# Performance work log

Measured on AMD Instinct MI355X. Metric: run time of the kernel, lower is better.

Reference implementation:

```python
import jax, jax.numpy as jnp
import numpy as np

B, C, H, W = 32, 320, 64, 64
CTX_DIM, CTX_HW = 1024, 16


def _conv3x3(x, w, b):
    # x: [b, cin, h, w], w: [cout, cin, 3, 3] (OIHW), stride 1, SAME padding
    y = jax.lax.conv_general_dilated(x, w, window_strides=(1, 1), padding='SAME',
                                     dimension_numbers=('NCHW', 'OIHW', 'NCHW'))
    return y + b[None, :, None, None]


def setup_inputs() -> dict:
    key = jax.random.key(0)
    ks = jax.random.split(key, 8)
    global_x = jax.random.normal(ks[0], (B, C, H, W), jnp.float32)
    context = jax.random.normal(ks[1], (B, CTX_HW * CTX_HW, CTX_DIM), jnp.float32)
    indicator = jax.random.randint(ks[2], (B, 2), 0, 2).astype(jnp.float32)
    # bbox = (x1, y1, x2, y2) normalized; keep boxes inside [0,1) so no sample
    # hits the torch try/except skip path, but sizes vary per sample.
    lo = jax.random.uniform(ks[3], (B, 2), minval=0.0, maxval=0.4)
    ext = jax.random.uniform(ks[4], (B, 2), minval=0.1, maxval=0.55)
    bbox = jnp.concatenate([lo, lo + ext], axis=1)
    # params (local_proj_out is zero-init in the source; we use small random
    # weights so the baseline is non-degenerate)
    w_in = jax.random.normal(ks[5], (C, CTX_DIM + 2, 3, 3), jnp.float32) * 0.02
    b_in = jnp.zeros((C,), jnp.float32)
    w_out = jax.random.normal(ks[6], (C, C, 3, 3), jnp.float32) * 0.02
    b_out = jnp.zeros((C,), jnp.float32)
    return {'global_x': global_x, 'context': context, 'indicator': indicator,
            'bbox': bbox, 'w_in': w_in, 'b_in': b_in, 'w_out': w_out, 'b_out': b_out}


def reference(global_x, context, indicator, bbox, w_in, b_in, w_out, b_out):
    b, c, h, w = global_x.shape
    # 'b (h w) c -> b c h w' with h=16
    ctx = context.reshape(b, CTX_HW, CTX_HW, -1).transpose(0, 3, 1, 2)
    ind_map = jnp.broadcast_to(indicator[:, :, None, None], (b, 2, CTX_HW, CTX_HW))
    ctx = jnp.concatenate([ctx, ind_map], axis=1)  # [b, ctx_dim+2, 16, 16]
    cx = _conv3x3(ctx, w_in, b_in)
    cx = cx * jax.nn.sigmoid(cx)                    # silu
    cx = _conv3x3(cx, w_out, b_out)                 # [b, c, 16, 16]
    # per-sample ROI nearest-resize + add, fully vectorized (torch loop body)
    bb = (bbox * h).astype(jnp.int32)               # truncation like .int()
    x1, y1 = bb[:, 0], bb[:, 1]
    x2 = jnp.maximum(bb[:, 2], x1 + 1)
    y2 = jnp.maximum(bb[:, 3], y1 + 1)
    # torch try/except skips samples where slice shapes mismatch (box off-grid)
    ok = (y2 <= h) & (x2 <= w) & (y1 >= 0) & (x1 >= 0)
    ys = jnp.arange(h)[None, :]
    xs = jnp.arange(w)[None, :]
    # nearest interpolation: src = floor(dst * in_size / out_size)
    src_y = jnp.clip(((ys - y1[:, None]) * CTX_HW) // (y2 - y1)[:, None], 0, CTX_HW - 1)
    src_x = jnp.clip(((xs - x1[:, None]) * CTX_HW) // (x2 - x1)[:, None], 0, CTX_HW - 1)
    vy = (ys >= y1[:, None]) & (ys < y2[:, None])   # [b, h]
    vx = (xs >= x1[:, None]) & (xs < x2[:, None])   # [b, w]
    bi = jnp.arange(b)[:, None, None]
    # gather per output pixel -> [b, h, w, c] -> [b, c, h, w]
    local = cx[bi, :, src_y[:, :, None], src_x[:, None, :]].transpose(0, 3, 1, 2)
    mask = (ok[:, None, None] & vy[:, :, None] & vx[:, None, :])[:, None]  # [b,1,h,w]
    return global_x + jnp.where(mask, local, jnp.zeros((), global_x.dtype))
```

## Files before the change

kernel.cpp:

```cpp
#include <hip/hip_runtime.h>
#include <cstddef>

#define BB 32
#define CC 320
#define HH 64
#define WW 64
#define CTX_HW 16
#define NPIX 256

typedef __attribute__((ext_vector_type(8))) short bf16x8;
typedef __attribute__((ext_vector_type(4))) float f32x4;

__device__ inline ushort f2bf(float x) {
  union { float f; unsigned u; } v; v.f = x;
  unsigned r = v.u + 0x7fff + ((v.u >> 16) & 1);
  return (ushort)(r >> 16);
}

__global__ __launch_bounds__(256) void cast_ctx(
    const float* __restrict__ ctx, const float* __restrict__ ind,
    ushort* __restrict__ ctxP, ushort* __restrict__ cx1P) {
  int b = blockIdx.x, p = blockIdx.y, t = threadIdx.x;
  ushort* orow = ctxP + ((size_t)b * 257 + p) * 1056;
  if (p < 256) {
    const float* irow = ctx + ((size_t)b * 256 + p) * 1024;
    float4 v = ((const float4*)irow)[t];
    ushort4 o;
    o.x = f2bf(v.x); o.y = f2bf(v.y); o.z = f2bf(v.z); o.w = f2bf(v.w);
    ((ushort4*)orow)[t] = o;
    if (t < 32) {
      float val = (t == 0) ? ind[b * 2] : (t == 1) ? ind[b * 2 + 1] : 0.0f;
      orow[1024 + t] = f2bf(val);
    }
  } else {
    ushort4 z = make_ushort4(0, 0, 0, 0);
    for (int i = t; i < 264; i += 256) ((ushort4*)orow)[i] = z;
    if (t < 80) ((ushort4*)(cx1P + ((size_t)b * 257 + 256) * 320))[t] = z;
  }
}

template <int KIN, int KP>
__global__ __launch_bounds__(256) void wt_tr(
    const float* __restrict__ w, ushort* __restrict__ wT) {
  __shared__ float wl[KIN * 9];
  int co = blockIdx.x, t = threadIdx.x;
  const float* wsrc = w + (size_t)co * KIN * 9;
  for (int i = t; i < KIN * 9; i += 256) wl[i] = wsrc[i];
  __syncthreads();
#pragma unroll
  for (int tap = 0; tap < 9; ++tap) {
    ushort* dst = wT + ((size_t)tap * 320 + co) * KP;
    for (int ci = t; ci < KP; ci += 256)
      dst[ci] = f2bf(ci < KIN ? wl[ci * 9 + tap] : 0.0f);
  }
}

__global__ __launch_bounds__(64) void prep_maps(
    const float* __restrict__ bbox, int* __restrict__ sy, int* __restrict__ sx) {
  int b = blockIdx.x;
  int t = threadIdx.x;
  int x1 = (int)(bbox[b * 4 + 0] * (float)HH);
  int y1 = (int)(bbox[b * 4 + 1] * (float)HH);
  int x2 = max((int)(bbox[b * 4 + 2] * (float)HH), x1 + 1);
  int y2 = max((int)(bbox[b * 4 + 3] * (float)HH), y1 + 1);
  bool ok = (y2 <= HH) && (x2 <= WW) && (y1 >= 0) && (x1 >= 0);
  int vy = -1, vx = -1;
  if (ok && t >= y1 && t < y2) vy = min(15, max(0, ((t - y1) * CTX_HW) / (y2 - y1)));
  if (ok && t >= x1 && t < x2) vx = min(15, max(0, ((t - x1) * CTX_HW) / (x2 - x1)));
  sy[b * 64 + t] = vy;
  sx[b * 64 + t] = vx;
}

template <int KP, int NCH, int KS>
__global__ __launch_bounds__(512, 4) void conv_part(
    const ushort* __restrict__ src, const ushort* __restrict__ wT,
    float* __restrict__ part) {
  constexpr int PL = 40;
  __shared__ ushort plane[257 * PL];

  int b = blockIdx.x;
  int co0 = blockIdx.y * 64;
  int z = blockIdx.z;
  int c0 = z * NCH / KS, c1 = (z + 1) * NCH / KS;
  int tid = threadIdx.x;
  int wid = tid >> 6, lane = tid & 63;
  int m = lane & 15, quad = lane >> 4;
  int mg = wid >> 1, ng = wid & 1;
  int y0 = mg * 4;
  int coA = co0 + ng * 32 + m;

  if (tid < PL) plane[256 * PL + tid] = 0;

  f32x4 acc[4][2];
#pragma unroll
  for (int i = 0; i < 4; ++i) {
    acc[i][0] = (f32x4)(0.0f);
    acc[i][1] = (f32x4)(0.0f);
  }

  const ushort* srcb = src + (size_t)b * 257 * KP;
  int row = tid >> 1, half = tid & 1;
  const ushort* gsrc = srcb + (size_t)row * KP + half * 16;
  ushort* lds_dst = plane + row * PL + half * 16;

  for (int cic = c0; cic < c1; ++cic) {
    __syncthreads();
    {
      const float4* g = (const float4*)(gsrc + cic * 32);
      float4 v0 = g[0];
      float4 v1 = g[1];
      ((float4*)lds_dst)[0] = v0;
      ((float4*)lds_dst)[1] = v1;
    }
    __syncthreads();
    const ushort* wb0 = wT + (size_t)coA * KP + cic * 32 + quad * 8;
    const ushort* wb1 = wb0 + (size_t)16 * KP;
#pragma unroll
    for (int dx = 0; dx < 3; ++dx) {
      int sxp = m + dx - 1;
      bool vx = (unsigned)sxp < 16u;
      bf16x8 af[6];
#pragma unroll
      for (int j = 0; j < 6; ++j) {
        int syr = y0 - 1 + j;
        bool v = vx && ((unsigned)syr < 16u);
        int ldsrow = v ? (syr * 16 + sxp) : 256;
        af[j] = *(const bf16x8*)(plane + ldsrow * PL + quad * 8);
      }
#pragma unroll
      for (int dy = 0; dy < 3; ++dy) {
        int tap = dy * 3 + dx;
        bf16x8 bf0 = *(const bf16x8*)(wb0 + (size_t)tap * 320 * KP);
        bf16x8 bf1 = *(const bf16x8*)(wb1 + (size_t)tap * 320 * KP);
#pragma unroll
        for (int mt = 0; mt < 4; ++mt) {
          acc[mt][0] = __builtin_amdgcn_mfma_f32_16x16x32_bf16(af[mt + dy], bf0,
                                                               acc[mt][0], 0, 0, 0);
          acc[mt][1] = __builtin_amdgcn_mfma_f32_16x16x32_bf16(af[mt + dy], bf1,
                                                               acc[mt][1], 0, 0, 0);
        }
      }
    }
  }

  float* pz = part + (size_t)z * BB * CC * NPIX + (size_t)b * CC * NPIX;
#pragma unroll
  for (int nt = 0; nt < 2; ++nt) {
    int co = coA + nt * 16;
#pragma unroll
    for (int mt = 0; mt < 4; ++mt) {
      *(f32x4*)(pz + (size_t)co * NPIX + (y0 + mt) * 16 + quad * 4) = acc[mt][nt];
    }
  }
}

__global__ __launch_bounds__(256) void combine1(
    const float* __restrict__ part, const float* __restrict__ bias,
    ushort* __restrict__ cx1P) {
  __shared__ float tile[64][65];
  int b = blockIdx.x, co0 = blockIdx.y * 64, px0 = blockIdx.z * 64;
  int t = threadIdx.x;
  int tx = t & 63, ty = t >> 6;
  const float* pb = part + ((size_t)b * CC + co0) * NPIX + px0 + tx;
  constexpr size_t KSTR = (size_t)BB * CC * NPIX;
#pragma unroll
  for (int i = 0; i < 16; ++i) {
    int cs = ty * 16 + i;
    const float* p = pb + (size_t)cs * NPIX;
    float s = p[0] + p[KSTR] + p[2 * KSTR] + p[3 * KSTR] + bias[co0 + cs];
    s = s / (1.0f + __expf(-s));
    tile[cs][tx] = s;
  }
  __syncthreads();
  int px = t >> 2, g = t & 3;
  ushort* dst = cx1P + ((size_t)b * 257 + px0 + px) * 320 + co0 + g * 16;
  ushort4 o[4];
#pragma unroll
  for (int i = 0; i < 16; ++i)
    ((ushort*)o)[i] = f2bf(tile[g * 16 + i][px]);
#pragma unroll
  for (int i = 0; i < 4; ++i) ((ushort4*)dst)[i] = o[i];
}

__global__ __launch_bounds__(256) void scatter_add(
    const float* __restrict__ gx, const float* __restrict__ p0,
    const float* __restrict__ p1, const float* __restrict__ b_out,
    const int* __restrict__ sy, const int* __restrict__ sx,
    float* __restrict__ out) {
  int blk = blockIdx.x;
  int part = blk & 3;
  int bc = blk >> 2;
  int b = bc / CC;
  float bo = b_out[bc % CC];
  int t = threadIdx.x;
  int e = part * 1024 + t * 4;
  int y = e >> 6, x0 = e & 63;
  size_t idx = (size_t)bc * 4096 + e;
  float4 g = *(const float4*)(gx + idx);
  int vy = sy[b * 64 + y];
  if (vy >= 0) {
    size_t base = (size_t)bc * NPIX + vy * 16;
    int v0 = sx[b * 64 + x0 + 0]; if (v0 >= 0) g.x += p0[base + v0] + p1[base + v0] + bo;
    int v1 = sx[b * 64 + x0 + 1]; if (v1 >= 0) g.y += p0[base + v1] + p1[base + v1] + bo;
    int v2 = sx[b * 64 + x0 + 2]; if (v2 >= 0) g.z += p0[base + v2] + p1[base + v2] + bo;
    int v3 = sx[b * 64 + x0 + 3]; if (v3 >= 0) g.w += p0[base + v3] + p1[base + v3] + bo;
  }
  *(float4*)(out + idx) = g;
}

extern "C" void kernel_launch(void* const* d_in, const int* in_sizes, int n_in,
                              void* d_out, int out_size, void* d_ws, size_t ws_size,
                              hipStream_t stream) {
  const float* gx    = (const float*)d_in[0];
  const float* ctx   = (const float*)d_in[1];
  const float* ind   = (const float*)d_in[2];
  const float* bbox  = (const float*)d_in[3];
  const float* w_in  = (const float*)d_in[4];
  const float* b_in  = (const float*)d_in[5];
  const float* w_out = (const float*)d_in[6];
  const float* b_out = (const float*)d_in[7];
  float* out = (float*)d_out;

  char* ws = (char*)d_ws;
  float* part1 = (float*)ws;
  float* part2 = (float*)ws;
  ws += (size_t)4 * BB * CC * NPIX * 4;
  ushort* ctxP = (ushort*)ws; ws += (size_t)BB * 257 * 1056 * 2;
  ushort* wT1  = (ushort*)ws; ws += (size_t)9 * 320 * 1056 * 2;
  ushort* wT2  = (ushort*)ws; ws += (size_t)9 * 320 * 320 * 2;
  ushort* cx1P = (ushort*)ws; ws += (size_t)BB * 257 * 320 * 2;
  int* sy = (int*)ws;         ws += BB * 64 * 4;
  int* sx = (int*)ws;

  cast_ctx<<<dim3(BB, 257), 256, 0, stream>>>(ctx, ind, ctxP, cx1P);
  wt_tr<1026, 1056><<<320, 256, 0, stream>>>(w_in, wT1);
  wt_tr<320, 320><<<320, 256, 0, stream>>>(w_out, wT2);
  prep_maps<<<BB, 64, 0, stream>>>(bbox, sy, sx);
  conv_part<1056, 33, 4><<<dim3(BB, 5, 4), 512, 0, stream>>>(ctxP, wT1, part1);
  combine1<<<dim3(BB, 5, 4), 256, 0, stream>>>(part1, b_in, cx1P);
  conv_part<320, 10, 2><<<dim3(BB, 5, 2), 512, 0, stream>>>(cx1P, wT2, part2);
  scatter_add<<<BB * CC * 4, 256, 0, stream>>>(gx, part2, part2 + (size_t)BB * CC * NPIX,
                                               b_out, sy, sx, out);
}
```

Baseline: 509.7 us.

## Fuse weight transposes, fold ROI map prep into scatter_add, shrink LDS pitch

Merges the two weight-transpose kernels into a single launch and moves bbox index-map computation into scatter_add. scatter_add now uses one block per (batch, channel), staging the summed conv partials plus bias and the index maps in shared memory. This cuts launches and repeated global gathers. The conv LDS row pitch is also reduced from 40 to 32 elements, which saves shared memory but may introduce bank conflicts on the A-fragment reads.

```diff
diff --git a/kernel.cpp b/kernel.cpp
--- a/kernel.cpp
+++ b/kernel.cpp
@@ -39,11 +39,9 @@
   }
 }
 
-template <int KIN, int KP>
-__global__ __launch_bounds__(256) void wt_tr(
-    const float* __restrict__ w, ushort* __restrict__ wT) {
-  __shared__ float wl[KIN * 9];
-  int co = blockIdx.x, t = threadIdx.x;
+__device__ inline void wt_body(const float* __restrict__ w, ushort* __restrict__ wT,
+                               int co, int KIN, int KP, float* wl) {
+  int t = threadIdx.x;
   const float* wsrc = w + (size_t)co * KIN * 9;
   for (int i = t; i < KIN * 9; i += 256) wl[i] = wsrc[i];
   __syncthreads();
@@ -55,27 +53,20 @@
   }
 }
 
-__global__ __launch_bounds__(64) void prep_maps(
-    const float* __restrict__ bbox, int* __restrict__ sy, int* __restrict__ sx) {
-  int b = blockIdx.x;
-  int t = threadIdx.x;
-  int x1 = (int)(bbox[b * 4 + 0] * (float)HH);
-  int y1 = (int)(bbox[b * 4 + 1] * (float)HH);
-  int x2 = max((int)(bbox[b * 4 + 2] * (float)HH), x1 + 1);
-  int y2 = max((int)(bbox[b * 4 + 3] * (float)HH), y1 + 1);
-  bool ok = (y2 <= HH) && (x2 <= WW) && (y1 >= 0) && (x1 >= 0);
-  int vy = -1, vx = -1;
-  if (ok && t >= y1 && t < y2) vy = min(15, max(0, ((t - y1) * CTX_HW) / (y2 - y1)));
-  if (ok && t >= x1 && t < x2) vx = min(15, max(0, ((t - x1) * CTX_HW) / (x2 - x1)));
-  sy[b * 64 + t] = vy;
-  sx[b * 64 + t] = vx;
+__global__ __launch_bounds__(256) void wt_both(
+    const float* __restrict__ w_in, const float* __restrict__ w_out,
+    ushort* __restrict__ wT1, ushort* __restrict__ wT2) {
+  __shared__ float wl[1026 * 9];
+  int blk = blockIdx.x;
+  if (blk < 320) wt_body(w_in, wT1, blk, 1026, 1056, wl);
+  else           wt_body(w_out, wT2, blk - 320, 320, 320, wl);
 }
 
 template <int KP, int NCH, int KS>
 __global__ __launch_bounds__(512, 4) void conv_part(
     const ushort* __restrict__ src, const ushort* __restrict__ wT,
     float* __restrict__ part) {
-  constexpr int PL = 40;
+  constexpr int PL = 32;
   __shared__ ushort plane[257 * PL];
 
   int b = blockIdx.x;
@@ -185,27 +176,46 @@
 __global__ __launch_bounds__(256) void scatter_add(
     const float* __restrict__ gx, const float* __restrict__ p0,
     const float* __restrict__ p1, const float* __restrict__ b_out,
-    const int* __restrict__ sy, const int* __restrict__ sx,
-    float* __restrict__ out) {
-  int blk = blockIdx.x;
-  int part = blk & 3;
-  int bc = blk >> 2;
-  int b = bc / CC;
-  float bo = b_out[bc % CC];
+    const float* __restrict__ bbox, float* __restrict__ out) {
+  __shared__ float lp[256];
+  __shared__ int sxs[64], sys[64];
+  int bc = blockIdx.x;
+  int b = bc / CC, c = bc - b * CC;
   int t = threadIdx.x;
-  int e = part * 1024 + t * 4;
-  int y = e >> 6, x0 = e & 63;
-  size_t idx = (size_t)bc * 4096 + e;
-  float4 g = *(const float4*)(gx + idx);
-  int vy = sy[b * 64 + y];
-  if (vy >= 0) {
-    size_t base = (size_t)bc * NPIX + vy * 16;
-    int v0 = sx[b * 64 + x0 + 0]; if (v0 >= 0) g.x += p0[base + v0] + p1[base + v0] + bo;
-    int v1 = sx[b * 64 + x0 + 1]; if (v1 >= 0) g.y += p0[base + v1] + p1[base + v1] + bo;
-    int v2 = sx[b * 64 + x0 + 2]; if (v2 >= 0) g.z += p0[base + v2] + p1[base + v2] + bo;
-    int v3 = sx[b * 64 + x0 + 3]; if (v3 >= 0) g.w += p0[base + v3] + p1[base + v3] + bo;
-  }
-  *(float4*)(out + idx) = g;
+
+  lp[t] = p0[(size_t)bc * NPIX + t] + p1[(size_t)bc * NPIX + t] + b_out[c];
+  if (t < 64) {
+    int x1 = (int)(bbox[b * 4 + 0] * (float)HH);
+    int y1 = (int)(bbox[b * 4 + 1] * (float)HH);
+    int x2 = max((int)(bbox[b * 4 + 2] * (float)HH), x1 + 1);
+    int y2 = max((int)(bbox[b * 4 + 3] * (float)HH), y1 + 1);
+    bool ok = (y2 <= HH) && (x2 <= WW) && (y1 >= 0) && (x1 >= 0);
+    int vy = -1, vx = -1;
+    if (ok && t >= y1 && t < y2) vy = min(15, max(0, ((t - y1) * CTX_HW) / (y2 - y1)));
+    if (ok && t >= x1 && t < x2) vx = min(15, max(0, ((t - x1) * CTX_HW) / (x2 - x1)));
+    sys[t] = vy;
+    sxs[t] = vx;
+  }
+  __syncthreads();
+
+  const float4* gx4 = (const float4*)(gx + (size_t)bc * 4096);
+  float4* out4 = (float4*)(out + (size_t)bc * 4096);
+#pragma unroll
+  for (int i = 0; i < 4; ++i) {
+    int j = i * 256 + t;
+    float4 g = gx4[j];
+    int y = j >> 4;
+    int x0 = (j & 15) * 4;
+    int vy = sys[y];
+    if (vy >= 0) {
+      const float* rowp = lp + vy * 16;
+      int v0 = sxs[x0 + 0]; if (v0 >= 0) g.x += rowp[v0];
+      int v1 = sxs[x0 + 1]; if (v1 >= 0) g.y += rowp[v1];
+      int v2 = sxs[x0 + 2]; if (v2 >= 0) g.z += rowp[v2];
+      int v3 = sxs[x0 + 3]; if (v3 >= 0) g.w += rowp[v3];
+    }
+    out4[j] = g;
+  }
 }
 
 extern "C" void kernel_launch(void* const* d_in, const int* in_sizes, int n_in,
@@ -229,16 +239,12 @@
   ushort* wT1  = (ushort*)ws; ws += (size_t)9 * 320 * 1056 * 2;
   ushort* wT2  = (ushort*)ws; ws += (size_t)9 * 320 * 320 * 2;
   ushort* cx1P = (ushort*)ws; ws += (size_t)BB * 257 * 320 * 2;
-  int* sy = (int*)ws;         ws += BB * 64 * 4;
-  int* sx = (int*)ws;
 
   cast_ctx<<<dim3(BB, 257), 256, 0, stream>>>(ctx, ind, ctxP, cx1P);
-  wt_tr<1026, 1056><<<320, 256, 0, stream>>>(w_in, wT1);
-  wt_tr<320, 320><<<320, 256, 0, stream>>>(w_out, wT2);
-  prep_maps<<<BB, 64, 0, stream>>>(bbox, sy, sx);
+  wt_both<<<640, 256, 0, stream>>>(w_in, w_out, wT1, wT2);
   conv_part<1056, 33, 4><<<dim3(BB, 5, 4), 512, 0, stream>>>(ctxP, wT1, part1);
   combine1<<<dim3(BB, 5, 4), 256, 0, stream>>>(part1, b_in, cx1P);
   conv_part<320, 10, 2><<<dim3(BB, 5, 2), 512, 0, stream>>>(cx1P, wT2, part2);
-  scatter_add<<<BB * CC * 4, 256, 0, stream>>>(gx, part2, part2 + (size_t)BB * CC * NPIX,
-                                               b_out, sy, sx, out);
-}
+  scatter_add<<<BB * CC, 256, 0, stream>>>(gx, part2, part2 + (size_t)BB * CC * NPIX,
+                                           b_out, bbox, out);
+}
```

After: 469.5 us. 7.9% less time.
